# Kernel optimization log

Hardware: AMD Instinct MI355X
Metric: run time of the kernel (lower is better)

The kernel has to match this reference:

```python
import math
import jax, jax.numpy as jnp
import numpy as np

N_HEADS = 16
D_EMBED = 1024
D_HEAD = D_EMBED // N_HEADS
B, S = 4, 2048


def setup_inputs() -> dict:
    key = jax.random.key(0)
    k1, k2, k3, k4, k5 = jax.random.split(key, 5)
    scale_in = 1.0 / math.sqrt(D_EMBED)
    return {
        "x": jax.random.normal(k1, (B, S, D_EMBED), dtype=jnp.float32),
        "w_in": jax.random.normal(k2, (3 * D_EMBED, D_EMBED), dtype=jnp.float32) * scale_in,
        "b_in": jax.random.normal(k3, (3 * D_EMBED,), dtype=jnp.float32) * 0.02,
        "w_out": jax.random.normal(k4, (D_EMBED, D_EMBED), dtype=jnp.float32) * scale_in,
        "b_out": jax.random.normal(k5, (D_EMBED,), dtype=jnp.float32) * 0.02,
        "causal_mask": 1,
    }


def reference(x, w_in, b_in, w_out, b_out, causal_mask):
    Bn, Sn, D = x.shape
    # fused QKV projection (torch Linear: x @ W.T + b)
    qkv = x @ w_in.T + b_in                       # (B, S, 3D)
    q, k, v = jnp.split(qkv, 3, axis=-1)
    def to_heads(t):
        return t.reshape(Bn, Sn, N_HEADS, D_HEAD).transpose(0, 2, 1, 3)  # (B,H,S,dh)
    q, k, v = to_heads(q), to_heads(k), to_heads(v)
    # manual scaled dot-product attention, full (B,H,S,S) scores
    scores = jnp.einsum("bhqd,bhkd->bhqk", q, k)
    if causal_mask:
        tri = jnp.triu(jnp.ones((Sn, Sn), dtype=bool), k=1)
        scores = jnp.where(tri, -jnp.inf, scores)
    scores = scores / math.sqrt(D_HEAD)
    weights = jax.nn.softmax(scores, axis=-1)
    out = jnp.einsum("bhqk,bhkd->bhqd", weights, v)  # (B,H,S,dh)
    out = out.transpose(0, 2, 1, 3).reshape(Bn, Sn, D)
    return out @ w_out.T + b_out
```

## Files before the change

kernel.cpp:

```cpp
#include <hip/hip_runtime.h>

typedef __bf16 bf16x8 __attribute__((ext_vector_type(8)));
typedef float  f32x4  __attribute__((ext_vector_type(4)));
typedef unsigned int uint;

__device__ inline unsigned short f2bf(float f) {
  union { float f; unsigned int u; } v; v.f = f;
  unsigned int u = v.u;
  unsigned int r = u + 0x7FFF + ((u >> 16) & 1);
  return (unsigned short)(r >> 16);
}

__device__ inline uint pack_bf16_rhu(float a, float b) {
  uint ua = __builtin_bit_cast(uint, a) + 0x8000u;
  uint ub = __builtin_bit_cast(uint, b) + 0x8000u;
  return __builtin_amdgcn_perm(ub, ua, 0x07060302u);
}

__device__ inline void load_lds16(const unsigned short* g, unsigned short* l) {
  __builtin_amdgcn_global_load_lds(
      (const __attribute__((address_space(1))) uint*)(g),
      (__attribute__((address_space(3))) uint*)(l), 16, 0, 0);
}

__device__ inline void cvt4(const float* in, unsigned short* out) {
  float4 f = *reinterpret_cast<const float4*>(in);
  ushort4 o;
  o.x = f2bf(f.x); o.y = f2bf(f.y); o.z = f2bf(f.z); o.w = f2bf(f.w);
  *reinterpret_cast<ushort4*>(out) = o;
}

__global__ void cvt_all(const float* __restrict__ x, const float* __restrict__ w_in,
                        const float* __restrict__ w_out,
                        unsigned short* __restrict__ x_bf,
                        unsigned short* __restrict__ w_in_bf,
                        unsigned short* __restrict__ w_out_bf) {
  const int n1 = 8192 * 1024, n2 = 3072 * 1024;
  int i = (blockIdx.x * blockDim.x + threadIdx.x) * 4;
  if (i < n1)            cvt4(x + i, x_bf + i);
  else if (i < n1 + n2)  cvt4(w_in + (i - n1), w_in_bf + (i - n1));
  else                   cvt4(w_out + (i - n1 - n2), w_out_bf + (i - n1 - n2));
}

template<bool OUT_BF16, bool VSPLIT>
__global__ __launch_bounds__(256) void gemm_bt128(
    const unsigned short* __restrict__ A,
    const unsigned short* __restrict__ B,
    const float* __restrict__ bias,
    void* __restrict__ Cout,
    unsigned short* __restrict__ vt,
    int M, int N, int K, int ldc, float scale, int ncut)
{
  __shared__ __attribute__((aligned(16))) unsigned short As[128 * 64];
  __shared__ __attribute__((aligned(16))) unsigned short Bs[128 * 64];

  const int t    = threadIdx.x;
  const int wave = t >> 6, lane = t & 63;
  const int l16  = lane & 15, quad = lane >> 4;
  const int wr = wave >> 1, wc = wave & 1;
  const int m0 = blockIdx.y * 128, n0 = blockIdx.x * 128;
  const int l8 = l16 & 7;

  f32x4 acc[4][4] = {};

  for (int k0 = 0; k0 < K; k0 += 64) {
#pragma unroll
    for (int i = 0; i < 4; ++i) {
      int chunk = i * 256 + t;
      int row = chunk >> 3, cb = chunk & 7;
      int gcb = cb ^ (row & 7);
      load_lds16(A + (size_t)(m0 + row) * K + k0 + gcb * 8, As + chunk * 8);
    }
#pragma unroll
    for (int i = 0; i < 4; ++i) {
      int chunk = i * 256 + t;
      int row = chunk >> 3, cb = chunk & 7;
      int gcb = cb ^ (row & 7);
      load_lds16(B + (size_t)(n0 + row) * K + k0 + gcb * 8, Bs + chunk * 8);
    }
    __syncthreads();
#pragma unroll
    for (int ks = 0; ks < 2; ++ks) {
      bf16x8 af[4], bfr[4];
#pragma unroll
      for (int mt = 0; mt < 4; ++mt)
        af[mt] = *(const bf16x8*)(As + (wr * 64 + mt * 16 + l16) * 64 +
                                  (((ks * 4 + quad) ^ l8) << 3));
#pragma unroll
      for (int nt = 0; nt < 4; ++nt)
        bfr[nt] = *(const bf16x8*)(Bs + (wc * 64 + nt * 16 + l16) * 64 +
                                   (((ks * 4 + quad) ^ l8) << 3));
#pragma unroll
      for (int mt = 0; mt < 4; ++mt)
#pragma unroll
        for (int nt = 0; nt < 4; ++nt)
          acc[mt][nt] = __builtin_amdgcn_mfma_f32_16x16x32_bf16(af[mt], bfr[nt], acc[mt][nt], 0, 0, 0);
    }
    __syncthreads();
  }

#pragma unroll
  for (int nt = 0; nt < 4; ++nt) {
    int col = n0 + wc * 64 + nt * 16 + l16;
    float bv = bias[col];
    float mlt = (col < ncut) ? scale : 1.0f;
#pragma unroll
    for (int mt = 0; mt < 4; ++mt) {
      int row0 = m0 + wr * 64 + mt * 16 + quad * 4;
      float v0 = (acc[mt][nt][0] + bv) * mlt;
      float v1 = (acc[mt][nt][1] + bv) * mlt;
      float v2 = (acc[mt][nt][2] + bv) * mlt;
      float v3 = (acc[mt][nt][3] + bv) * mlt;
      if (VSPLIT && col >= 2048) {
        int d = col - 2048, h = d >> 6, dd = d & 63;
        int bb = row0 >> 11, s = row0 & 2047;
        uint2 w;
        w.x = pack_bf16_rhu(v0, v1);
        w.y = pack_bf16_rhu(v2, v3);
        *(uint2*)(vt + ((size_t)((bb * 16 + h) * 64 + dd) * 2048 + s)) = w;
      } else {
#pragma unroll
        for (int r = 0; r < 4; ++r) {
          float v = (r == 0) ? v0 : (r == 1) ? v1 : (r == 2) ? v2 : v3;
          if (OUT_BF16)
            ((unsigned short*)Cout)[(size_t)(row0 + r) * ldc + col] = f2bf(v);
          else
            ((float*)Cout)[(size_t)(row0 + r) * ldc + col] = v;
        }
      }
    }
  }
}

__global__ __launch_bounds__(256) void attn(
    const unsigned short* __restrict__ qkv2,
    const unsigned short* __restrict__ vt,
    unsigned short* __restrict__ y,
    const int* __restrict__ flag)
{
  __shared__ __attribute__((aligned(16))) unsigned short Qs[128 * 64];
  __shared__ __attribute__((aligned(16))) unsigned short Ks[2][64 * 64];
  __shared__ __attribute__((aligned(16))) unsigned short Vs[2][64 * 64];

  const int t    = threadIdx.x;
  const int wave = t >> 6, lane = t & 63;
  const int l16  = lane & 15, quad = lane >> 4;
  const int l8   = l16 & 7;
  const int idx  = blockIdx.x;
  const int bh   = idx & 63;
  const int pair = idx >> 6;
  const int b = bh >> 4, h = bh & 15;
  const int causal = flag[0];

  const unsigned short* Qg  = qkv2 + (size_t)b * 2048 * 2048 + h * 64;
  const unsigned short* Kg  = Qg + 1024;
  const unsigned short* Vtg = vt + (size_t)bh * 64 * 2048;

  const int sr = t >> 2, sg = (t & 3) * 2;
  const int slot0 = sr * 64 + (((sg    ) ^ (sr & 7)) << 3);
  const int slot1 = sr * 64 + (((sg + 1) ^ (sr & 7)) << 3);
  const int kr = t >> 3, kg = t & 7;
  const int kslot = kr * 64 + ((kg ^ (kr & 7)) << 3);

  unsigned short* Ps = Qs;

  for (int half = 0; half < 2; ++half) {
    const int qt = half ? pair : (15 - pair);
    const int q0 = qt * 128;
    const int jmax = causal ? 2 * qt + 1 : 31;

    const unsigned short* kptr = Kg + (size_t)kr * 2048 + kg * 8;
    const unsigned short* vptr = Vtg + (size_t)kr * 2048 + kg * 8;
    uint4 kreg0 = *(const uint4*)kptr;
    uint4 kreg1 = *(const uint4*)(kptr + 32 * 2048);
    uint4 vreg0 = *(const uint4*)vptr;
    uint4 vreg1 = *(const uint4*)(vptr + 32 * 2048);
    {
      const unsigned short* src  = Qg + (size_t)(q0 + sr) * 2048 + sg * 8;
      const unsigned short* src2 = src + 64 * 2048;
      *(uint4*)(Qs + slot0)        = *(const uint4*)src;
      *(uint4*)(Qs + slot1)        = *(const uint4*)(src + 8);
      *(uint4*)(Qs + slot0 + 4096) = *(const uint4*)src2;
      *(uint4*)(Qs + slot1 + 4096) = *(const uint4*)(src2 + 8);
    }
    __syncthreads();
    bf16x8 qf[2][2];
#pragma unroll
    for (int g = 0; g < 2; ++g)
#pragma unroll
      for (int ks = 0; ks < 2; ++ks)
        qf[g][ks] = *(const bf16x8*)(Qs + (wave * 32 + g * 16 + l16) * 64 +
                                     (((ks * 4 + quad) ^ l8) << 3));
    __syncthreads();

    *(uint4*)(Ks[0] + kslot)        = kreg0;
    *(uint4*)(Ks[0] + kslot + 2048) = kreg1;
    *(uint4*)(Vs[0] + kslot)        = vreg0;
    *(uint4*)(Vs[0] + kslot + 2048) = vreg1;
    kptr += 64 * 2048;
    vptr += 64;
    if (jmax > 0) {
      kreg0 = *(const uint4*)kptr;
      kreg1 = *(const uint4*)(kptr + 32 * 2048);
      vreg0 = *(const uint4*)vptr;
      vreg1 = *(const uint4*)(vptr + 32 * 2048);
    }
    __syncthreads();

    f32x4 ot[2][4] = {};
    float l_lane[2] = {0.f, 0.f};
    const int q_glob = q0 + wave * 32 + l16;
    const int wq_max = q0 + wave * 32 + 31;

    for (int j = 0; j <= jmax; ++j) {
      const int cur = j & 1;
      if (j < jmax) {
        *(uint4*)(Ks[cur ^ 1] + kslot)        = kreg0;
        *(uint4*)(Ks[cur ^ 1] + kslot + 2048) = kreg1;
        *(uint4*)(Vs[cur ^ 1] + kslot)        = vreg0;
        *(uint4*)(Vs[cur ^ 1] + kslot + 2048) = vreg1;
        if (j + 1 < jmax) {
          kptr += 64 * 2048;
          vptr += 64;
          kreg0 = *(const uint4*)kptr;
          kreg1 = *(const uint4*)(kptr + 32 * 2048);
          vreg0 = *(const uint4*)vptr;
          vreg1 = *(const uint4*)(vptr + 32 * 2048);
        }
      }

      const bool active = !causal || ((j << 6) <= wq_max);
      if (active) {
        f32x4 st[2][4] = {};
        __builtin_amdgcn_s_setprio(1);
#pragma unroll
        for (int ks = 0; ks < 2; ++ks) {
#pragma unroll
          for (int mt = 0; mt < 4; ++mt) {
            bf16x8 kf = *(const bf16x8*)(Ks[cur] + (mt * 16 + l16) * 64 +
                                         (((ks * 4 + quad) ^ l8) << 3));
            st[0][mt] = __builtin_amdgcn_mfma_f32_16x16x32_bf16(kf, qf[0][ks], st[0][mt], 0, 0, 0);
            st[1][mt] = __builtin_amdgcn_mfma_f32_16x16x32_bf16(kf, qf[1][ks], st[1][mt], 0, 0, 0);
          }
        }
        __builtin_amdgcn_s_setprio(0);

        const int kv0 = j << 6;
#pragma unroll
        for (int g = 0; g < 2; ++g) {
          const int qg = q_glob + g * 16;
          const bool diag = (causal != 0) && (kv0 + 63 > qg);
          const int prow = (wave * 32 + g * 16 + l16) * 64;
#pragma unroll
          for (int mt = 0; mt < 4; ++mt) {
            float p[4];
#pragma unroll
            for (int r = 0; r < 4; ++r) {
              float pv = __builtin_amdgcn_exp2f(st[g][mt][r]);
              if (diag) {
                int kv = kv0 + mt * 16 + quad * 4 + r;
                if (kv > qg) pv = 0.f;
              }
              p[r] = pv;
            }
            l_lane[g] += (p[0] + p[1]) + (p[2] + p[3]);
            uint2 w;
            w.x = pack_bf16_rhu(p[0], p[1]);
            w.y = pack_bf16_rhu(p[2], p[3]);
            *(uint2*)(Ps + prow +
                      ((((mt * 2 + (quad >> 1)) ^ l8) << 3) + (quad & 1) * 4)) = w;
          }
        }
        __threadfence_block();

        __builtin_amdgcn_s_setprio(1);
#pragma unroll
        for (int ks = 0; ks < 2; ++ks) {
          const int gofs = ((ks * 4 + quad) ^ l8) << 3;
          bf16x8 pf0 = *(const bf16x8*)(Ps + (wave * 32 + l16) * 64 + gofs);
          bf16x8 pf1 = *(const bf16x8*)(Ps + (wave * 32 + 16 + l16) * 64 + gofs);
#pragma unroll
          for (int mt = 0; mt < 4; ++mt) {
            bf16x8 vf = *(const bf16x8*)(Vs[cur] + (mt * 16 + l16) * 64 + gofs);
            ot[0][mt] = __builtin_amdgcn_mfma_f32_16x16x32_bf16(vf, pf0, ot[0][mt], 0, 0, 0);
            ot[1][mt] = __builtin_amdgcn_mfma_f32_16x16x32_bf16(vf, pf1, ot[1][mt], 0, 0, 0);
          }
        }
        __builtin_amdgcn_s_setprio(0);
      }
      __syncthreads();
    }

#pragma unroll
    for (int g = 0; g < 2; ++g) {
      float l = l_lane[g];
      l += __shfl_xor(l, 16);
      l += __shfl_xor(l, 32);
      float inv = 1.f / l;
      const int prow = (wave * 32 + g * 16 + l16) * 64;
#pragma unroll
      for (int mt = 0; mt < 4; ++mt) {
        uint2 w;
        w.x = pack_bf16_rhu(ot[g][mt][0] * inv, ot[g][mt][1] * inv);
        w.y = pack_bf16_rhu(ot[g][mt][2] * inv, ot[g][mt][3] * inv);
        *(uint2*)(Ps + prow +
                  ((((mt * 2 + (quad >> 1)) ^ l8) << 3) + (quad & 1) * 4)) = w;
      }
    }
    __syncthreads();
    {
      size_t base0 = ((size_t)b * 2048 + q0 + sr) * 1024 + h * 64 + sg * 8;
      size_t base1 = base0 + (size_t)64 * 1024;
      *(uint4*)(y + base0)     = *(const uint4*)(Ps + slot0);
      *(uint4*)(y + base0 + 8) = *(const uint4*)(Ps + slot1);
      *(uint4*)(y + base1)     = *(const uint4*)(Ps + slot0 + 4096);
      *(uint4*)(y + base1 + 8) = *(const uint4*)(Ps + slot1 + 4096);
    }
    __syncthreads();
  }
}

extern "C" void kernel_launch(void* const* d_in, const int* in_sizes, int n_in,
                              void* d_out, int out_size, void* d_ws, size_t ws_size,
                              hipStream_t stream) {
  const float* x     = (const float*)d_in[0];
  const float* w_in  = (const float*)d_in[1];
  const float* b_in  = (const float*)d_in[2];
  const float* w_out = (const float*)d_in[3];
  const float* b_out = (const float*)d_in[4];
  const int*   cmask = (const int*)d_in[5];

  char* ws = (char*)d_ws;
  unsigned short* x_bf     = (unsigned short*)(ws);
  unsigned short* w_in_bf  = (unsigned short*)(ws + 16777216);
  unsigned short* w_out_bf = (unsigned short*)(ws + 23068672);
  unsigned short* qkv2_bf  = (unsigned short*)(ws + 25165824);
  unsigned short* vt_bf    = (unsigned short*)(ws + 58720256);
  unsigned short* y_bf     = (unsigned short*)(ws + 75497472);

  const int ntot = (8192 + 3072 + 1024) * 1024;
  cvt_all<<<dim3(ntot / 4 / 256), 256, 0, stream>>>(x, w_in, w_out, x_bf, w_in_bf, w_out_bf);

  gemm_bt128<true, true><<<dim3(24, 64), 256, 0, stream>>>(
      x_bf, w_in_bf, b_in, qkv2_bf, vt_bf, 8192, 3072, 1024, 2048,
      0.18033688011112042f, 1024);

  attn<<<dim3(512), 256, 0, stream>>>(qkv2_bf, vt_bf, y_bf, cmask);

  gemm_bt128<false, false><<<dim3(8, 64), 256, 0, stream>>>(
      y_bf, w_out_bf, b_out, d_out, nullptr, 8192, 1024, 1024, 1024, 1.0f, 0);
}
```

Measured before the change: 262.0 us.

## Use 512-thread attention blocks over 256-row query tiles instead of paired 128-row tiles

The attention kernel moves from 256-thread blocks that each handle two balanced 128-row query tiles in sequence to 512-thread blocks that each handle one 256-row query tile. Each staged 64-row K/V tile is now shared by eight waves instead of four, roughly halving K/V global loads and LDS staging per query row, and each thread loads one vector per tile instead of two. The cost is that the causal load balancing from pairing short and long tiles is lost. Block work now varies widely (4 to 32 KV iterations), which is only partly offset by launching the longest tiles first. LDS per block also grows, which may lower how many blocks fit on a CU at once.

```diff
diff --git a/kernel.cpp b/kernel.cpp
--- a/kernel.cpp
+++ b/kernel.cpp
@@ -132,13 +132,13 @@
   }
 }
 
-__global__ __launch_bounds__(256) void attn(
+__global__ __launch_bounds__(512) void attn(
     const unsigned short* __restrict__ qkv2,
     const unsigned short* __restrict__ vt,
     unsigned short* __restrict__ y,
     const int* __restrict__ flag)
 {
-  __shared__ __attribute__((aligned(16))) unsigned short Qs[128 * 64];
+  __shared__ __attribute__((aligned(16))) unsigned short Qs[256 * 64];
   __shared__ __attribute__((aligned(16))) unsigned short Ks[2][64 * 64];
   __shared__ __attribute__((aligned(16))) unsigned short Vs[2][64 * 64];
 
@@ -148,9 +148,12 @@
   const int l8   = l16 & 7;
   const int idx  = blockIdx.x;
   const int bh   = idx & 63;
-  const int pair = idx >> 6;
+  const int g8   = idx >> 6;
+  const int qt   = (g8 < 4) ? (7 - g8) : (g8 - 4);
   const int b = bh >> 4, h = bh & 15;
   const int causal = flag[0];
+  const int q0 = qt * 256;
+  const int jmax = causal ? 4 * qt + 3 : 31;
 
   const unsigned short* Qg  = qkv2 + (size_t)b * 2048 * 2048 + h * 64;
   const unsigned short* Kg  = Qg + 1024;
@@ -164,159 +167,142 @@
 
   unsigned short* Ps = Qs;
 
-  for (int half = 0; half < 2; ++half) {
-    const int qt = half ? pair : (15 - pair);
-    const int q0 = qt * 128;
-    const int jmax = causal ? 2 * qt + 1 : 31;
-
-    const unsigned short* kptr = Kg + (size_t)kr * 2048 + kg * 8;
-    const unsigned short* vptr = Vtg + (size_t)kr * 2048 + kg * 8;
-    uint4 kreg0 = *(const uint4*)kptr;
-    uint4 kreg1 = *(const uint4*)(kptr + 32 * 2048);
-    uint4 vreg0 = *(const uint4*)vptr;
-    uint4 vreg1 = *(const uint4*)(vptr + 32 * 2048);
-    {
-      const unsigned short* src  = Qg + (size_t)(q0 + sr) * 2048 + sg * 8;
-      const unsigned short* src2 = src + 64 * 2048;
-      *(uint4*)(Qs + slot0)        = *(const uint4*)src;
-      *(uint4*)(Qs + slot1)        = *(const uint4*)(src + 8);
-      *(uint4*)(Qs + slot0 + 4096) = *(const uint4*)src2;
-      *(uint4*)(Qs + slot1 + 4096) = *(const uint4*)(src2 + 8);
+  const unsigned short* kptr = Kg + (size_t)kr * 2048 + kg * 8;
+  const unsigned short* vptr = Vtg + (size_t)kr * 2048 + kg * 8;
+  uint4 kreg = *(const uint4*)kptr;
+  uint4 vreg = *(const uint4*)vptr;
+  {
+    const unsigned short* src  = Qg + (size_t)(q0 + sr) * 2048 + sg * 8;
+    const unsigned short* src2 = src + (size_t)128 * 2048;
+    *(uint4*)(Qs + slot0)        = *(const uint4*)src;
+    *(uint4*)(Qs + slot1)        = *(const uint4*)(src + 8);
+    *(uint4*)(Qs + slot0 + 8192) = *(const uint4*)src2;
+    *(uint4*)(Qs + slot1 + 8192) = *(const uint4*)(src2 + 8);
+  }
+  __syncthreads();
+  bf16x8 qf[2][2];
+#pragma unroll
+  for (int g = 0; g < 2; ++g)
+#pragma unroll
+    for (int ks = 0; ks < 2; ++ks)
+      qf[g][ks] = *(const bf16x8*)(Qs + (wave * 32 + g * 16 + l16) * 64 +
+                                   (((ks * 4 + quad) ^ l8) << 3));
+  __syncthreads();
+
+  *(uint4*)(Ks[0] + kslot) = kreg;
+  *(uint4*)(Vs[0] + kslot) = vreg;
+  kptr += 64 * 2048;
+  vptr += 64;
+  if (jmax > 0) {
+    kreg = *(const uint4*)kptr;
+    vreg = *(const uint4*)vptr;
+  }
+  __syncthreads();
+
+  f32x4 ot[2][4] = {};
+  float l_lane[2] = {0.f, 0.f};
+  const int q_glob = q0 + wave * 32 + l16;
+  const int wq_max = q0 + wave * 32 + 31;
+
+  for (int j = 0; j <= jmax; ++j) {
+    const int cur = j & 1;
+    if (j < jmax) {
+      *(uint4*)(Ks[cur ^ 1] + kslot) = kreg;
+      *(uint4*)(Vs[cur ^ 1] + kslot) = vreg;
+      if (j + 1 < jmax) {
+        kptr += 64 * 2048;
+        vptr += 64;
+        kreg = *(const uint4*)kptr;
+        vreg = *(const uint4*)vptr;
+      }
+    }
+
+    const bool active = !causal || ((j << 6) <= wq_max);
+    if (active) {
+      f32x4 st[2][4] = {};
+      __builtin_amdgcn_s_setprio(1);
+#pragma unroll
+      for (int ks = 0; ks < 2; ++ks) {
+#pragma unroll
+        for (int mt = 0; mt < 4; ++mt) {
+          bf16x8 kf = *(const bf16x8*)(Ks[cur] + (mt * 16 + l16) * 64 +
+                                       (((ks * 4 + quad) ^ l8) << 3));
+          st[0][mt] = __builtin_amdgcn_mfma_f32_16x16x32_bf16(kf, qf[0][ks], st[0][mt], 0, 0, 0);
+          st[1][mt] = __builtin_amdgcn_mfma_f32_16x16x32_bf16(kf, qf[1][ks], st[1][mt], 0, 0, 0);
+        }
+      }
+      __builtin_amdgcn_s_setprio(0);
+
+      const int kv0 = j << 6;
+#pragma unroll
+      for (int g = 0; g < 2; ++g) {
+        const int qg = q_glob + g * 16;
+        const bool diag = (causal != 0) && (kv0 + 63 > qg);
+        const int prow = (wave * 32 + g * 16 + l16) * 64;
+#pragma unroll
+        for (int mt = 0; mt < 4; ++mt) {
+          float p[4];
+#pragma unroll
+          for (int r = 0; r < 4; ++r) {
+            float pv = __builtin_amdgcn_exp2f(st[g][mt][r]);
+            if (diag) {
+              int kv = kv0 + mt * 16 + quad * 4 + r;
+              if (kv > qg) pv = 0.f;
+            }
+            p[r] = pv;
+          }
+          l_lane[g] += (p[0] + p[1]) + (p[2] + p[3]);
+          uint2 w;
+          w.x = pack_bf16_rhu(p[0], p[1]);
+          w.y = pack_bf16_rhu(p[2], p[3]);
+          *(uint2*)(Ps + prow +
+                    ((((mt * 2 + (quad >> 1)) ^ l8) << 3) + (quad & 1) * 4)) = w;
+        }
+      }
+      __threadfence_block();
+
+      __builtin_amdgcn_s_setprio(1);
+#pragma unroll
+      for (int ks = 0; ks < 2; ++ks) {
+        const int gofs = ((ks * 4 + quad) ^ l8) << 3;
+        bf16x8 pf0 = *(const bf16x8*)(Ps + (wave * 32 + l16) * 64 + gofs);
+        bf16x8 pf1 = *(const bf16x8*)(Ps + (wave * 32 + 16 + l16) * 64 + gofs);
+#pragma unroll
+        for (int mt = 0; mt < 4; ++mt) {
+          bf16x8 vf = *(const bf16x8*)(Vs[cur] + (mt * 16 + l16) * 64 + gofs);
+          ot[0][mt] = __builtin_amdgcn_mfma_f32_16x16x32_bf16(vf, pf0, ot[0][mt], 0, 0, 0);
+          ot[1][mt] = __builtin_amdgcn_mfma_f32_16x16x32_bf16(vf, pf1, ot[1][mt], 0, 0, 0);
+        }
+      }
+      __builtin_amdgcn_s_setprio(0);
     }
     __syncthreads();
-    bf16x8 qf[2][2];
-#pragma unroll
-    for (int g = 0; g < 2; ++g)
-#pragma unroll
-      for (int ks = 0; ks < 2; ++ks)
-        qf[g][ks] = *(const bf16x8*)(Qs + (wave * 32 + g * 16 + l16) * 64 +
-                                     (((ks * 4 + quad) ^ l8) << 3));
-    __syncthreads();
-
-    *(uint4*)(Ks[0] + kslot)        = kreg0;
-    *(uint4*)(Ks[0] + kslot + 2048) = kreg1;
-    *(uint4*)(Vs[0] + kslot)        = vreg0;
-    *(uint4*)(Vs[0] + kslot + 2048) = vreg1;
-    kptr += 64 * 2048;
-    vptr += 64;
-    if (jmax > 0) {
-      kreg0 = *(const uint4*)kptr;
-      kreg1 = *(const uint4*)(kptr + 32 * 2048);
-      vreg0 = *(const uint4*)vptr;
-      vreg1 = *(const uint4*)(vptr + 32 * 2048);
-    }
-    __syncthreads();
-
-    f32x4 ot[2][4] = {};
-    float l_lane[2] = {0.f, 0.f};
-    const int q_glob = q0 + wave * 32 + l16;
-    const int wq_max = q0 + wave * 32 + 31;
-
-    for (int j = 0; j <= jmax; ++j) {
-      const int cur = j & 1;
-      if (j < jmax) {
-        *(uint4*)(Ks[cur ^ 1] + kslot)        = kreg0;
-        *(uint4*)(Ks[cur ^ 1] + kslot + 2048) = kreg1;
-        *(uint4*)(Vs[cur ^ 1] + kslot)        = vreg0;
-        *(uint4*)(Vs[cur ^ 1] + kslot + 2048) = vreg1;
-        if (j + 1 < jmax) {
-          kptr += 64 * 2048;
-          vptr += 64;
-          kreg0 = *(const uint4*)kptr;
-          kreg1 = *(const uint4*)(kptr + 32 * 2048);
-          vreg0 = *(const uint4*)vptr;
-          vreg1 = *(const uint4*)(vptr + 32 * 2048);
-        }
-      }
-
-      const bool active = !causal || ((j << 6) <= wq_max);
-      if (active) {
-        f32x4 st[2][4] = {};
-        __builtin_amdgcn_s_setprio(1);
-#pragma unroll
-        for (int ks = 0; ks < 2; ++ks) {
-#pragma unroll
-          for (int mt = 0; mt < 4; ++mt) {
-            bf16x8 kf = *(const bf16x8*)(Ks[cur] + (mt * 16 + l16) * 64 +
-                                         (((ks * 4 + quad) ^ l8) << 3));
-            st[0][mt] = __builtin_amdgcn_mfma_f32_16x16x32_bf16(kf, qf[0][ks], st[0][mt], 0, 0, 0);
-            st[1][mt] = __builtin_amdgcn_mfma_f32_16x16x32_bf16(kf, qf[1][ks], st[1][mt], 0, 0, 0);
-          }
-        }
-        __builtin_amdgcn_s_setprio(0);
-
-        const int kv0 = j << 6;
-#pragma unroll
-        for (int g = 0; g < 2; ++g) {
-          const int qg = q_glob + g * 16;
-          const bool diag = (causal != 0) && (kv0 + 63 > qg);
-          const int prow = (wave * 32 + g * 16 + l16) * 64;
-#pragma unroll
-          for (int mt = 0; mt < 4; ++mt) {
-            float p[4];
-#pragma unroll
-            for (int r = 0; r < 4; ++r) {
-              float pv = __builtin_amdgcn_exp2f(st[g][mt][r]);
-              if (diag) {
-                int kv = kv0 + mt * 16 + quad * 4 + r;
-                if (kv > qg) pv = 0.f;
-              }
-              p[r] = pv;
-            }
-            l_lane[g] += (p[0] + p[1]) + (p[2] + p[3]);
-            uint2 w;
-            w.x = pack_bf16_rhu(p[0], p[1]);
-            w.y = pack_bf16_rhu(p[2], p[3]);
-            *(uint2*)(Ps + prow +
-                      ((((mt * 2 + (quad >> 1)) ^ l8) << 3) + (quad & 1) * 4)) = w;
-          }
-        }
-        __threadfence_block();
-
-        __builtin_amdgcn_s_setprio(1);
-#pragma unroll
-        for (int ks = 0; ks < 2; ++ks) {
-          const int gofs = ((ks * 4 + quad) ^ l8) << 3;
-          bf16x8 pf0 = *(const bf16x8*)(Ps + (wave * 32 + l16) * 64 + gofs);
-          bf16x8 pf1 = *(const bf16x8*)(Ps + (wave * 32 + 16 + l16) * 64 + gofs);
-#pragma unroll
-          for (int mt = 0; mt < 4; ++mt) {
-            bf16x8 vf = *(const bf16x8*)(Vs[cur] + (mt * 16 + l16) * 64 + gofs);
-            ot[0][mt] = __builtin_amdgcn_mfma_f32_16x16x32_bf16(vf, pf0, ot[0][mt], 0, 0, 0);
-            ot[1][mt] = __builtin_amdgcn_mfma_f32_16x16x32_bf16(vf, pf1, ot[1][mt], 0, 0, 0);
-          }
-        }
-        __builtin_amdgcn_s_setprio(0);
-      }
-      __syncthreads();
-    }
-
-#pragma unroll
-    for (int g = 0; g < 2; ++g) {
-      float l = l_lane[g];
-      l += __shfl_xor(l, 16);
-      l += __shfl_xor(l, 32);
-      float inv = 1.f / l;
-      const int prow = (wave * 32 + g * 16 + l16) * 64;
-#pragma unroll
-      for (int mt = 0; mt < 4; ++mt) {
-        uint2 w;
-        w.x = pack_bf16_rhu(ot[g][mt][0] * inv, ot[g][mt][1] * inv);
-        w.y = pack_bf16_rhu(ot[g][mt][2] * inv, ot[g][mt][3] * inv);
-        *(uint2*)(Ps + prow +
-                  ((((mt * 2 + (quad >> 1)) ^ l8) << 3) + (quad & 1) * 4)) = w;
-      }
-    }
-    __syncthreads();
-    {
-      size_t base0 = ((size_t)b * 2048 + q0 + sr) * 1024 + h * 64 + sg * 8;
-      size_t base1 = base0 + (size_t)64 * 1024;
-      *(uint4*)(y + base0)     = *(const uint4*)(Ps + slot0);
-      *(uint4*)(y + base0 + 8) = *(const uint4*)(Ps + slot1);
-      *(uint4*)(y + base1)     = *(const uint4*)(Ps + slot0 + 4096);
-      *(uint4*)(y + base1 + 8) = *(const uint4*)(Ps + slot1 + 4096);
-    }
-    __syncthreads();
+  }
+
+#pragma unroll
+  for (int g = 0; g < 2; ++g) {
+    float l = l_lane[g];
+    l += __shfl_xor(l, 16);
+    l += __shfl_xor(l, 32);
+    float inv = 1.f / l;
+    const int prow = (wave * 32 + g * 16 + l16) * 64;
+#pragma unroll
+    for (int mt = 0; mt < 4; ++mt) {
+      uint2 w;
+      w.x = pack_bf16_rhu(ot[g][mt][0] * inv, ot[g][mt][1] * inv);
+      w.y = pack_bf16_rhu(ot[g][mt][2] * inv, ot[g][mt][3] * inv);
+      *(uint2*)(Ps + prow +
+                ((((mt * 2 + (quad >> 1)) ^ l8) << 3) + (quad & 1) * 4)) = w;
+    }
+  }
+  __syncthreads();
+  {
+    size_t base0 = ((size_t)b * 2048 + q0 + sr) * 1024 + h * 64 + sg * 8;
+    size_t base1 = base0 + (size_t)128 * 1024;
+    *(uint4*)(y + base0)     = *(const uint4*)(Ps + slot0);
+    *(uint4*)(y + base0 + 8) = *(const uint4*)(Ps + slot1);
+    *(uint4*)(y + base1)     = *(const uint4*)(Ps + slot0 + 8192);
+    *(uint4*)(y + base1 + 8) = *(const uint4*)(Ps + slot1 + 8192);
   }
 }
 
@@ -345,7 +331,7 @@
       x_bf, w_in_bf, b_in, qkv2_bf, vt_bf, 8192, 3072, 1024, 2048,
       0.18033688011112042f, 1024);
 
-  attn<<<dim3(512), 256, 0, stream>>>(qkv2_bf, vt_bf, y_bf, cmask);
+  attn<<<dim3(512), 512, 0, stream>>>(qkv2_bf, vt_bf, y_bf, cmask);
 
   gemm_bt128<false, false><<<dim3(8, 64), 256, 0, stream>>>(
       y_bf, w_out_bf, b_out, d_out, nullptr, 8192, 1024, 1024, 1024, 1.0f, 0);
```

Measured after the change: 258.8 us. Within noise of the previous version (-1.2%).
